# Kernel tuning notes

Measured on AMD Instinct MI355X. Metric: run time of the kernel, lower is better.

Reference implementation:

```python
import jax, jax.numpy as jnp
import numpy as np

D = 512      # input_size == per-head embed_size (wide attention)
H = 8        # num_attn_heads


def setup_inputs() -> dict:
    key = jax.random.key(0)
    ks = jax.random.split(key, 8)
    B, S = 2, 2048
    scale = 1.0 / np.sqrt(D)
    return {
        "Xin_q": jax.random.normal(ks[0], (B, S, D), dtype=jnp.float32),
        "Xin_k": jax.random.normal(ks[1], (B, S, D), dtype=jnp.float32),
        "Xin_v": jax.random.normal(ks[2], (B, S, D), dtype=jnp.float32),
        # per-head projection weights, stored as [H, D_in, D_out] (bias-free)
        "Wq": jax.random.normal(ks[3], (H, D, D), dtype=jnp.float32) * scale,
        "Wk": jax.random.normal(ks[4], (H, D, D), dtype=jnp.float32) * scale,
        "Wv": jax.random.normal(ks[5], (H, D, D), dtype=jnp.float32) * scale,
        # output projection: concat(H*D) -> D, with bias
        "Wz": jax.random.normal(ks[6], (H * D, D), dtype=jnp.float32) * (1.0 / np.sqrt(H * D)),
        "bz": jax.random.normal(ks[7], (D,), dtype=jnp.float32) * 0.01,
    }


def reference(Xin_q, Xin_k, Xin_v, Wq, Wk, Wv, Wz, bz):
    B, Sq, _ = Xin_q.shape
    inv4 = 1.0 / (D ** 0.25)  # each of Q and K scaled by embed_size**(1/4)
    # project all heads at once: [B,H,S,D]
    q = jnp.einsum("bsd,hde->bhse", Xin_q, Wq) * inv4
    k = jnp.einsum("bsd,hde->bhse", Xin_k, Wk) * inv4
    v = jnp.einsum("bsd,hde->bhse", Xin_v, Wv)
    attn = jax.nn.softmax(jnp.einsum("bhqe,bhke->bhqk", q, k), axis=-1)
    z = jnp.einsum("bhqk,bhke->bhqe", attn, v)        # [B,H,S,D]
    # concat heads along last dim (head-major order matches torch.cat over the head loop)
    z = jnp.transpose(z, (0, 2, 1, 3)).reshape(B, Sq, H * D)
    out = z @ Wz + bz                                  # [B,S,D]
    attn_avg = jnp.mean(attn, axis=1)                  # [B,Sq,Skv]
    return out, attn_avg
```

## Files before the change

kernel.cpp:

```cpp
#include <hip/hip_runtime.h>
#include <math.h>

#define BB 2
#define SS 2048
#define D_ 512
#define H_ 8
#define MS (BB * SS)
#define HD (H_ * D_)

typedef short bf16x8 __attribute__((ext_vector_type(8)));
typedef float f32x4 __attribute__((ext_vector_type(4)));

__device__ inline unsigned short f2bf(float f) {
    union { float f; unsigned u; } x{f};
    unsigned r = x.u + 0x7fff + ((x.u >> 16) & 1);
    return (unsigned short)(r >> 16);
}
__device__ inline float bf2f(unsigned short u) {
    union { unsigned u; float f; } x{(unsigned)u << 16};
    return x.f;
}

constexpr size_t SZ_X   = (size_t)MS * D_ * 2;
constexpr size_t SZ_W   = (size_t)H_ * D_ * D_ * 2;
constexpr size_t SZ_WZ  = (size_t)HD * D_ * 2;
constexpr size_t SZ_QK  = (size_t)H_ * MS * D_ * 2;
constexpr size_t SZ_SC  = (size_t)H_ * BB * SS * SS * 2;
constexpr size_t SZ_Z   = (size_t)MS * HD * 2;
constexpr size_t SZ_OP  = (size_t)2 * MS * D_ * 4;
constexpr size_t SZ_LV  = (size_t)H_ * BB * SS * 4;
constexpr size_t OFF_XQ  = 0;
constexpr size_t OFF_XK  = OFF_XQ + SZ_X;
constexpr size_t OFF_XV  = OFF_XK + SZ_X;
constexpr size_t OFF_WQT = OFF_XV + SZ_X;
constexpr size_t OFF_WKT = OFF_WQT + SZ_W;
constexpr size_t OFF_WVT = OFF_WKT + SZ_W;
constexpr size_t OFF_WZT = OFF_WVT + SZ_W;
constexpr size_t OFF_QB  = OFF_WZT + SZ_WZ;
constexpr size_t OFF_KB  = OFF_QB + SZ_QK;
constexpr size_t OFF_VT  = OFF_KB + SZ_QK;
constexpr size_t OFF_SC  = OFF_VT + SZ_QK;
constexpr size_t OFF_Z   = OFF_SC + SZ_SC;
constexpr size_t OFF_OP  = OFF_Z + SZ_Z;
constexpr size_t OFF_LV  = OFF_OP + SZ_OP;
constexpr size_t WS_TOTAL = OFF_LV + SZ_LV;
__device__ __align__(256) unsigned char g_ws[WS_TOTAL];

__device__ inline void gl2lds16(const unsigned short* g, unsigned short* l) {
    __builtin_amdgcn_global_load_lds(
        (const __attribute__((address_space(1))) void*)g,
        (__attribute__((address_space(3))) void*)l, 16, 0, 0);
}

#define BAR() __builtin_amdgcn_s_barrier()
#define PRIO1() __builtin_amdgcn_s_setprio(1)
#define PRIO0() __builtin_amdgcn_s_setprio(0)
#define VMW4() asm volatile("s_waitcnt vmcnt(4)" ::: "memory")
#define VMW0() asm volatile("s_waitcnt vmcnt(0)" ::: "memory")

__device__ __forceinline__ void rd_a(const unsigned short* p, int qm, int o0, int o1,
                                     bf16x8 (&Af)[8]) {
#pragma unroll
    for (int fi = 0; fi < 4; fi++) {
        Af[2 * fi]     = *(const bf16x8*)(p + (qm * 64 + fi * 16) * 64 + o0);
        Af[2 * fi + 1] = *(const bf16x8*)(p + (qm * 64 + fi * 16) * 64 + o1);
    }
}
__device__ __forceinline__ void rd_b(const unsigned short* p, int qn, int o0, int o1,
                                     bf16x8 (&Bf)[4]) {
#pragma unroll
    for (int fj = 0; fj < 2; fj++) {
        Bf[2 * fj]     = *(const bf16x8*)(p + (qn * 32 + fj * 16) * 64 + o0);
        Bf[2 * fj + 1] = *(const bf16x8*)(p + (qn * 32 + fj * 16) * 64 + o1);
    }
}
__device__ __forceinline__ void mma_q(int qm, int qn, const bf16x8 (&Af)[8],
                                      const bf16x8 (&Bf)[4], f32x4 (&acc)[8][4]) {
#pragma unroll
    for (int fi = 0; fi < 4; fi++)
#pragma unroll
        for (int fj = 0; fj < 2; fj++) {
            acc[qm * 4 + fi][qn * 2 + fj] = __builtin_amdgcn_mfma_f32_16x16x32_bf16(
                Af[2 * fi], Bf[2 * fj], acc[qm * 4 + fi][qn * 2 + fj], 0, 0, 0);
            acc[qm * 4 + fi][qn * 2 + fj] = __builtin_amdgcn_mfma_f32_16x16x32_bf16(
                Af[2 * fi + 1], Bf[2 * fj + 1], acc[qm * 4 + fi][qn * 2 + fj], 0, 0, 0);
        }
}

__global__ __launch_bounds__(512, 2) void gemm256_k(
    const unsigned short* __restrict__ A, const unsigned short* __restrict__ B,
    unsigned short* __restrict__ C, int K, int ldA, int ldB, int ldC,
    long sA1, long sA2, long sB1, long sB2, long sC1, long sC2, int d2,
    float alpha, int doExp, const float* __restrict__ rowScale, long sR1, long sR2)
{
    __shared__ unsigned short LA[2][256 * 64];
    __shared__ unsigned short LB[2][256 * 64];
    const int gx = gridDim.x, gy = gridDim.y, gz = gridDim.z;
    int bx, by, bz;
    if (((gy * gz) & 7) == 0) {
        const long L = blockIdx.x + (long)gx * (blockIdx.y + (long)gy * blockIdx.z);
        const int d = (int)(L & 7);
        const long s = L >> 3;
        bx = (int)(s % gx);
        const long yz = d + 8 * (s / gx);
        by = (int)(yz % gy);
        bz = (int)(yz / gy);
    } else {
        bx = blockIdx.x; by = blockIdx.y; bz = blockIdx.z;
    }
    const int z1 = bz / d2, z2 = bz % d2;
    A += z1 * sA1 + z2 * sA2;
    B += z1 * sB1 + z2 * sB2;
    const long cOff = z1 * sC1 + z2 * sC2;
    const long rsOff = z1 * sR1 + z2 * sR2;
    const int m0 = by * 256, n0 = bx * 256;
    const int tid = threadIdx.x;
    const int w = tid >> 6, l = tid & 63;
    const int wm = w >> 2, wn = w & 3;

    const int sr = l >> 3;
    const int sq = (l & 7) ^ sr;
    const unsigned short* gA = A + (long)(m0 + w * 16 + sr) * ldA + sq * 8;
    const unsigned short* gB = B + (long)(n0 + w * 16 + sr) * ldB + sq * 8;

    const int q = l >> 4, sl = l & 7;
    const int o0 = (q ^ sl) * 8;
    const int o1 = ((q + 4) ^ sl) * 8;
    const unsigned short* pa0 = &LA[0][(wm * 128 + (l & 15)) * 64];
    const unsigned short* pa1 = &LA[1][(wm * 128 + (l & 15)) * 64];
    const unsigned short* pb0 = &LB[0][(wn * 64 + (l & 15)) * 64];
    const unsigned short* pb1 = &LB[1][(wn * 64 + (l & 15)) * 64];

    const int nK2 = K >> 7;
    f32x4 acc[8][4] = {};
    bf16x8 Af[8], Bf0[4], Bf1[4];

#define STG_A(bufi, half, t) do { \
    gl2lds16(gA + (long)((half) * 128) * ldA + (long)(t) * 64, \
             &LA[bufi][((half) * 128 + w * 16) * 64]); \
    gl2lds16(gA + (long)((half) * 128 + 8) * ldA + (long)(t) * 64, \
             &LA[bufi][((half) * 128 + w * 16 + 8) * 64]); } while (0)
#define STG_B(bufi, half, t) do { \
    gl2lds16(gB + (long)((half) * 128) * ldB + (long)(t) * 64, \
             &LB[bufi][((half) * 128 + w * 16) * 64]); \
    gl2lds16(gB + (long)((half) * 128 + 8) * ldB + (long)(t) * 64, \
             &LB[bufi][((half) * 128 + w * 16 + 8) * 64]); } while (0)

    STG_A(0, 0, 0); STG_A(0, 1, 0);
    STG_B(0, 0, 0); STG_B(0, 1, 0);
    STG_B(1, 0, 1); STG_B(1, 1, 1);
    VMW4();
    BAR();

    for (int u = 0; u < nK2; ++u) {
        const int t1 = 2 * u + 1, t2 = 2 * u + 2, t3 = 2 * u + 3;
        const bool have = (u + 1 < nK2);
        rd_a(pa0, 0, o0, o1, Af);
        rd_b(pb0, 0, o0, o1, Bf0);
        STG_A(1, 0, t1);
        BAR(); PRIO1(); mma_q(0, 0, Af, Bf0, acc); PRIO0(); BAR();
        rd_b(pb0, 1, o0, o1, Bf1);
        STG_A(1, 1, t1);
        BAR(); PRIO1(); mma_q(0, 1, Af, Bf1, acc); PRIO0(); BAR();
        rd_a(pa0, 1, o0, o1, Af);
        if (have) STG_B(0, 0, t2);
        BAR(); PRIO1(); mma_q(1, 1, Af, Bf1, acc); PRIO0(); BAR();
        if (have) STG_B(0, 1, t2);
        BAR(); PRIO1(); mma_q(1, 0, Af, Bf0, acc); PRIO0();
        if (have) VMW4(); else VMW0();
        BAR();
        rd_a(pa1, 0, o0, o1, Af);
        rd_b(pb1, 0, o0, o1, Bf0);
        if (have) STG_A(0, 0, t2);
        BAR(); PRIO1(); mma_q(0, 0, Af, Bf0, acc); PRIO0(); BAR();
        rd_b(pb1, 1, o0, o1, Bf1);
        if (have) STG_A(0, 1, t2);
        BAR(); PRIO1(); mma_q(0, 1, Af, Bf1, acc); PRIO0(); BAR();
        rd_a(pa1, 1, o0, o1, Af);
        if (have) STG_B(1, 0, t3);
        BAR(); PRIO1(); mma_q(1, 1, Af, Bf1, acc); PRIO0(); BAR();
        if (have) STG_B(1, 1, t3);
        BAR(); PRIO1(); mma_q(1, 0, Af, Bf0, acc); PRIO0();
        if (have) VMW4(); else VMW0();
        BAR();
    }
#undef STG_A
#undef STG_B

    const int rowB = m0 + wm * 128 + q * 4;
    const int colB = n0 + wn * 64 + (l & 15);
    unsigned short* Cp = C + cOff;
#pragma unroll
    for (int mi = 0; mi < 8; mi++) {
#pragma unroll
        for (int rg = 0; rg < 4; rg++) {
            const int row = rowB + mi * 16 + rg;
            const float rs = rowScale ? rowScale[rsOff + row] : 1.0f;
#pragma unroll
            for (int nj = 0; nj < 4; nj++) {
                float v = alpha * acc[mi][nj][rg];
                if (doExp) v = __expf(v);
                Cp[(long)row * ldC + colB + nj * 16] = f2bf(v * rs);
            }
        }
    }
}

__global__ __launch_bounds__(256) void gemm_bt_k(
    const unsigned short* __restrict__ A, const unsigned short* __restrict__ B,
    void* __restrict__ Cv, int K, int ldA, int ldB, int ldC,
    long sA1, long sA2, long sB1, long sB2, long sC1, long sC2, int d2,
    float alpha, const float* __restrict__ bias, int outBf16, int doExp,
    const float* __restrict__ rowScale, long sR1, long sR2)
{
    __shared__ unsigned short As[128 * 64];
    __shared__ unsigned short Bs[128 * 64];
    const int gx = gridDim.x, gy = gridDim.y, gz = gridDim.z;
    int bx, by, bz;
    if (((gy * gz) & 7) == 0) {
        const long L = blockIdx.x + (long)gx * (blockIdx.y + (long)gy * blockIdx.z);
        const int d = (int)(L & 7);
        const long s = L >> 3;
        bx = (int)(s % gx);
        const long yz = d + 8 * (s / gx);
        by = (int)(yz % gy);
        bz = (int)(yz / gy);
    } else {
        bx = blockIdx.x; by = blockIdx.y; bz = blockIdx.z;
    }
    const int z1 = bz / d2, z2 = bz % d2;
    A += z1 * sA1 + z2 * sA2;
    B += z1 * sB1 + z2 * sB2;
    const long cOff = z1 * sC1 + z2 * sC2;
    const long rsOff = z1 * sR1 + z2 * sR2;
    const int m0 = by * 128, n0 = bx * 128;
    const int tid = threadIdx.x;
    const int w = tid >> 6, l = tid & 63;

    const int sr = l >> 3;
    const int sq = (l & 7) ^ sr;
    const unsigned short* ga = A + (long)(m0 + w * 32 + sr) * ldA + sq * 8;
    const unsigned short* gb = B + (long)(n0 + w * 32 + sr) * ldB + sq * 8;
    unsigned short* laA = As + w * 2048;
    unsigned short* laB = Bs + w * 2048;

    const int wm = w >> 1, wn = w & 1;
    const int q = l >> 4;
    const int sl = l & 7;
    const int mA = wm * 64 + (l & 15);
    const int nB = wn * 64 + (l & 15);
    const int s0 = ((q) ^ sl) * 8;
    const int s1 = ((q + 4) ^ sl) * 8;
    const unsigned short* pa0 = As + mA * 64 + s0;
    const unsigned short* pa1 = As + mA * 64 + s1;
    const unsigned short* pb0 = Bs + nB * 64 + s0;
    const unsigned short* pb1 = Bs + nB * 64 + s1;

    f32x4 acc[4][4] = {};
    for (int kk = 0; kk < K; kk += 64) {
#pragma unroll
        for (int i = 0; i < 4; i++) {
            gl2lds16(ga + (long)i * 8 * ldA, laA + i * 512);
            gl2lds16(gb + (long)i * 8 * ldB, laB + i * 512);
        }
        ga += 64; gb += 64;
        __syncthreads();
        bf16x8 af[4], bf[4];
#pragma unroll
        for (int i = 0; i < 4; i++) {
            af[i] = *(const bf16x8*)(pa0 + i * 1024);
            bf[i] = *(const bf16x8*)(pb0 + i * 1024);
        }
#pragma unroll
        for (int mi = 0; mi < 4; mi++)
#pragma unroll
            for (int ni = 0; ni < 4; ni++)
                acc[mi][ni] = __builtin_amdgcn_mfma_f32_16x16x32_bf16(
                    af[mi], bf[ni], acc[mi][ni], 0, 0, 0);
#pragma unroll
        for (int i = 0; i < 4; i++) {
            af[i] = *(const bf16x8*)(pa1 + i * 1024);
            bf[i] = *(const bf16x8*)(pb1 + i * 1024);
        }
#pragma unroll
        for (int mi = 0; mi < 4; mi++)
#pragma unroll
            for (int ni = 0; ni < 4; ni++)
                acc[mi][ni] = __builtin_amdgcn_mfma_f32_16x16x32_bf16(
                    af[mi], bf[ni], acc[mi][ni], 0, 0, 0);
        __syncthreads();
    }

    const int rowB = m0 + wm * 64 + q * 4;
    const int colB = n0 + wn * 64 + (l & 15);
    if (outBf16) {
        unsigned short* C = (unsigned short*)Cv + cOff;
#pragma unroll
        for (int mi = 0; mi < 4; mi++) {
#pragma unroll
            for (int rg = 0; rg < 4; rg++) {
                const int row = rowB + mi * 16 + rg;
                const float rs = rowScale ? rowScale[rsOff + row] : 1.0f;
#pragma unroll
                for (int ni = 0; ni < 4; ni++) {
                    float v = alpha * acc[mi][ni][rg];
                    if (doExp) v = __expf(v);
                    C[(long)row * ldC + colB + ni * 16] = f2bf(v * rs);
                }
            }
        }
    } else {
        float* C = (float*)Cv + cOff;
#pragma unroll
        for (int ni = 0; ni < 4; ni++) {
            const int col = colB + ni * 16;
            const float bs = bias ? bias[col] : 0.f;
#pragma unroll
            for (int mi = 0; mi < 4; mi++)
#pragma unroll
                for (int rg = 0; rg < 4; rg++)
                    C[(long)(rowB + mi * 16 + rg) * ldC + col] =
                        alpha * acc[mi][ni][rg] + bs;
        }
    }
}

__global__ __launch_bounds__(256) void cvt3_k(
    const float* __restrict__ i0, const float* __restrict__ i1, const float* __restrict__ i2,
    unsigned short* __restrict__ o0, unsigned short* __restrict__ o1,
    unsigned short* __restrict__ o2, long n4)
{
    const float* in = blockIdx.z == 0 ? i0 : (blockIdx.z == 1 ? i1 : i2);
    unsigned short* out = blockIdx.z == 0 ? o0 : (blockIdx.z == 1 ? o1 : o2);
    long i = (long)blockIdx.x * 256 + threadIdx.x;
    if (i >= n4) return;
    float4 v = ((const float4*)in)[i];
    ushort4 o;
    o.x = f2bf(v.x); o.y = f2bf(v.y); o.z = f2bf(v.z); o.w = f2bf(v.w);
    ((ushort4*)out)[i] = o;
}

__global__ __launch_bounds__(256) void transcvt3_k(
    const float* __restrict__ i0, const float* __restrict__ i1, const float* __restrict__ i2,
    unsigned short* __restrict__ o0, unsigned short* __restrict__ o1,
    unsigned short* __restrict__ o2)
{
    __shared__ float t[32][33];
    const int zt = blockIdx.z >> 3, h = blockIdx.z & 7;
    const float* in = (zt == 0 ? i0 : (zt == 1 ? i1 : i2)) + (long)h * D_ * D_;
    unsigned short* out = (zt == 0 ? o0 : (zt == 1 ? o1 : o2)) + (long)h * D_ * D_;
    const int r0 = blockIdx.y * 32, c0 = blockIdx.x * 32;
    const int tr = threadIdx.x >> 5, tc = threadIdx.x & 31;
#pragma unroll
    for (int i = 0; i < 4; i++)
        t[tr + i * 8][tc] = in[(long)(r0 + tr + i * 8) * D_ + c0 + tc];
    __syncthreads();
#pragma unroll
    for (int i = 0; i < 4; i++)
        out[(long)(c0 + tr + i * 8) * D_ + r0 + tc] = f2bf(t[tc][tr + i * 8]);
}

__global__ __launch_bounds__(256) void transcvt_k(
    const float* __restrict__ in, unsigned short* __restrict__ out, int R, int C)
{
    __shared__ float t[32][33];
    const int r0 = blockIdx.y * 32, c0 = blockIdx.x * 32;
    const int tr = threadIdx.x >> 5, tc = threadIdx.x & 31;
#pragma unroll
    for (int i = 0; i < 4; i++)
        t[tr + i * 8][tc] = in[(long)(r0 + tr + i * 8) * C + c0 + tc];
    __syncthreads();
#pragma unroll
    for (int i = 0; i < 4; i++)
        out[(long)(c0 + tr + i * 8) * R + r0 + tc] = f2bf(t[tc][tr + i * 8]);
}

__device__ inline float wred_sum(float v) {
#pragma unroll
    for (int o = 32; o; o >>= 1) v += __shfl_down(v, o);
    return v;
}
__global__ __launch_bounds__(256) void sumavg_k(
    const unsigned short* __restrict__ E, float* __restrict__ avg,
    float* __restrict__ linv)
{
    const int blk = blockIdx.x;
    const int b = blk >> 11, s = blk & (SS - 1);
    const int tid = threadIdx.x;
    __shared__ float red[4];
    float av[8] = {};
    const int t0 = tid * 8;
    for (int h = 0; h < H_; h++) {
        const long rowOff = ((long)(h * BB + b) * SS + s) * SS + t0;
        const ushort4 u0 = *(const ushort4*)(E + rowOff);
        const ushort4 u1 = *(const ushort4*)(E + rowOff + 4);
        float vals[8] = {bf2f(u0.x), bf2f(u0.y), bf2f(u0.z), bf2f(u0.w),
                         bf2f(u1.x), bf2f(u1.y), bf2f(u1.z), bf2f(u1.w)};
        float sum = 0.f;
#pragma unroll
        for (int i = 0; i < 8; i++) sum += vals[i];
        float wsum = wred_sum(sum);
        if ((tid & 63) == 0) red[tid >> 6] = wsum;
        __syncthreads();
        sum = red[0] + red[1] + red[2] + red[3];
        __syncthreads();
        const float inv = 1.0f / sum;
        if (tid == 0) linv[(long)(h * BB + b) * SS + s] = inv;
        const float invH = inv * 0.125f;
#pragma unroll
        for (int i = 0; i < 8; i++) av[i] += vals[i] * invH;
    }
    const long aOff = ((long)b * SS + s) * SS + t0;
    float4 a0 = {av[0], av[1], av[2], av[3]};
    float4 a1 = {av[4], av[5], av[6], av[7]};
    *(float4*)(avg + aOff) = a0;
    *(float4*)(avg + aOff + 4) = a1;
}

__global__ __launch_bounds__(256) void addbias_k(
    const float* __restrict__ p0, const float* __restrict__ p1,
    const float* __restrict__ bz, float* __restrict__ out)
{
    const long n4 = (long)MS * D_ / 4;
    long i = (long)blockIdx.x * 256 + threadIdx.x;
    if (i >= n4) return;
    const int col4 = (int)((i * 4) & (D_ - 1));
    float4 a = ((const float4*)p0)[i];
    float4 b = ((const float4*)p1)[i];
    float4 c = *(const float4*)(bz + col4);
    float4 o = {a.x + b.x + c.x, a.y + b.y + c.y, a.z + b.z + c.z, a.w + b.w + c.w};
    ((float4*)out)[i] = o;
}

extern "C" void kernel_launch(void* const* d_in, const int* in_sizes, int n_in,
                              void* d_out, int out_size, void* d_ws, size_t ws_size,
                              hipStream_t stream)
{
    const float* Xq = (const float*)d_in[0];
    const float* Xk = (const float*)d_in[1];
    const float* Xv = (const float*)d_in[2];
    const float* Wq = (const float*)d_in[3];
    const float* Wk = (const float*)d_in[4];
    const float* Wv = (const float*)d_in[5];
    const float* Wz = (const float*)d_in[6];
    const float* bz = (const float*)d_in[7];

    float* out      = (float*)d_out;
    float* attn_avg = out + (long)MS * D_;

    unsigned char* ws = nullptr;
    (void)hipGetSymbolAddress((void**)&ws, HIP_SYMBOL(g_ws));
    unsigned short* Xbq = (unsigned short*)(ws + OFF_XQ);
    unsigned short* Xbk = (unsigned short*)(ws + OFF_XK);
    unsigned short* Xbv = (unsigned short*)(ws + OFF_XV);
    unsigned short* Wqt = (unsigned short*)(ws + OFF_WQT);
    unsigned short* Wkt = (unsigned short*)(ws + OFF_WKT);
    unsigned short* Wvt = (unsigned short*)(ws + OFF_WVT);
    unsigned short* Wzt = (unsigned short*)(ws + OFF_WZT);
    unsigned short* qb  = (unsigned short*)(ws + OFF_QB);
    unsigned short* vT  = (unsigned short*)(ws + OFF_VT);
    unsigned short* scb = (unsigned short*)(ws + OFF_SC);
    unsigned short* zal = (unsigned short*)(ws + OFF_Z);
    float*          opp = (float*)(ws + OFF_OP);
    float*          linv = (float*)(ws + OFF_LV);

    const float inv4 = 1.0f / powf((float)D_, 0.25f);

    const long n4x = (long)MS * D_ / 4;
    cvt3_k<<<dim3((n4x + 255) / 256, 1, 3), 256, 0, stream>>>(
        Xq, Xk, Xv, Xbq, Xbk, Xbv, n4x);
    transcvt3_k<<<dim3(16, 16, 24), 256, 0, stream>>>(Wq, Wk, Wv, Wqt, Wkt, Wvt);
    transcvt_k<<<dim3(16, 128, 1), 256, 0, stream>>>(Wz, Wzt, HD, D_);

    gemm256_k<<<dim3(2, 16, 16), 512, 0, stream>>>(
        Xbq, Wqt, qb, D_, D_, D_, D_,
        (long)MS * D_, 0, (long)H_ * D_ * D_, (long)D_ * D_,
        (long)H_ * MS * D_, (long)MS * D_, 8, inv4, 0, nullptr, 0, 0);
    gemm256_k<<<dim3(8, 2, 16), 512, 0, stream>>>(
        Wvt, Xbv, vT, D_, D_, D_, SS,
        (long)D_ * D_, 0, 0, (long)SS * D_, (long)2 * D_ * SS, (long)D_ * SS, 2,
        1.0f, 0, nullptr, 0, 0);

    gemm256_k<<<dim3(8, 8, 16), 512, 0, stream>>>(
        qb, qb + (long)H_ * MS * D_, scb, D_, D_, D_, SS,
        (long)MS * D_, (long)SS * D_, (long)MS * D_, (long)SS * D_,
        (long)2 * SS * SS, (long)SS * SS, 2, 1.0f, 1, nullptr, 0, 0);

    sumavg_k<<<dim3(BB * SS), 256, 0, stream>>>(scb, attn_avg, linv);

    gemm256_k<<<dim3(2, 8, 16), 512, 0, stream>>>(
        scb, vT, zal, SS, SS, SS, HD,
        (long)2 * SS * SS, (long)SS * SS, (long)2 * D_ * SS, (long)D_ * SS,
        512, (long)SS * HD, 2, 1.0f, 0,
        linv, (long)BB * SS, (long)SS);

    gemm_bt_k<<<dim3(4, 32, 2), 256, 0, stream>>>(
        zal, Wzt, opp, HD / 2, HD, HD, D_,
        0, 2048, 0, 2048, 0, (long)MS * D_, 2, 1.0f, nullptr, 0, 0, nullptr, 0, 0);
    const long n4o = (long)MS * D_ / 4;
    addbias_k<<<dim3((n4o + 255) / 256), 256, 0, stream>>>(
        opp, opp + (long)MS * D_, bz, out);
}
```

Before: 476.1 us.

## Double-buffer GEMM register fragments to overlap LDS reads with MFMA

Splits the A and B register fragments into two sets each, so LDS reads for the next quarter-tile are issued before the current MFMA block. The first fragments are prefetched before the loop and the next iteration's are loaded at the end. Each phase now has one barrier instead of two, and sched_barrier fences keep the compiler from reordering across phases. The aim is to hide LDS latency and cut barrier stalls, at the cost of more VGPRs, which could reduce occupancy, and a more delicate barrier ordering around buffer reuse.

```diff
diff --git a/kernel.cpp b/kernel.cpp
--- a/kernel.cpp
+++ b/kernel.cpp
@@ -55,6 +55,7 @@
 #define BAR() __builtin_amdgcn_s_barrier()
 #define PRIO1() __builtin_amdgcn_s_setprio(1)
 #define PRIO0() __builtin_amdgcn_s_setprio(0)
+#define SCHED0() __builtin_amdgcn_sched_barrier(0)
 #define VMW4() asm volatile("s_waitcnt vmcnt(4)" ::: "memory")
 #define VMW0() asm volatile("s_waitcnt vmcnt(0)" ::: "memory")
 
@@ -133,7 +134,7 @@
 
     const int nK2 = K >> 7;
     f32x4 acc[8][4] = {};
-    bf16x8 Af[8], Bf0[4], Bf1[4];
+    bf16x8 AfX[8], AfY[8], BfP[4], BfQ[4];
 
 #define STG_A(bufi, half, t) do { \
     gl2lds16(gA + (long)((half) * 128) * ldA + (long)(t) * 64, \
@@ -151,37 +152,55 @@
     STG_B(1, 0, 1); STG_B(1, 1, 1);
     VMW4();
     BAR();
+    rd_a(pa0, 0, o0, o1, AfX);
+    rd_b(pb0, 0, o0, o1, BfP);
 
     for (int u = 0; u < nK2; ++u) {
         const int t1 = 2 * u + 1, t2 = 2 * u + 2, t3 = 2 * u + 3;
         const bool have = (u + 1 < nK2);
-        rd_a(pa0, 0, o0, o1, Af);
-        rd_b(pb0, 0, o0, o1, Bf0);
+        rd_b(pb0, 1, o0, o1, BfQ);
         STG_A(1, 0, t1);
-        BAR(); PRIO1(); mma_q(0, 0, Af, Bf0, acc); PRIO0(); BAR();
-        rd_b(pb0, 1, o0, o1, Bf1);
+        SCHED0();
+        PRIO1(); mma_q(0, 0, AfX, BfP, acc); PRIO0();
+        BAR();
+        rd_a(pa0, 1, o0, o1, AfY);
         STG_A(1, 1, t1);
-        BAR(); PRIO1(); mma_q(0, 1, Af, Bf1, acc); PRIO0(); BAR();
-        rd_a(pa0, 1, o0, o1, Af);
+        SCHED0();
+        PRIO1(); mma_q(0, 1, AfX, BfQ, acc); PRIO0();
+        BAR();
         if (have) STG_B(0, 0, t2);
-        BAR(); PRIO1(); mma_q(1, 1, Af, Bf1, acc); PRIO0(); BAR();
+        SCHED0();
+        PRIO1(); mma_q(1, 1, AfY, BfQ, acc); PRIO0();
+        BAR();
         if (have) STG_B(0, 1, t2);
-        BAR(); PRIO1(); mma_q(1, 0, Af, Bf0, acc); PRIO0();
         if (have) VMW4(); else VMW0();
         BAR();
-        rd_a(pa1, 0, o0, o1, Af);
-        rd_b(pb1, 0, o0, o1, Bf0);
+        rd_a(pa1, 0, o0, o1, AfX);
+        SCHED0();
+        PRIO1(); mma_q(1, 0, AfY, BfP, acc); PRIO0();
+        rd_b(pb1, 0, o0, o1, BfP);
+        BAR();
+        rd_b(pb1, 1, o0, o1, BfQ);
         if (have) STG_A(0, 0, t2);
-        BAR(); PRIO1(); mma_q(0, 0, Af, Bf0, acc); PRIO0(); BAR();
-        rd_b(pb1, 1, o0, o1, Bf1);
+        SCHED0();
+        PRIO1(); mma_q(0, 0, AfX, BfP, acc); PRIO0();
+        BAR();
+        rd_a(pa1, 1, o0, o1, AfY);
         if (have) STG_A(0, 1, t2);
-        BAR(); PRIO1(); mma_q(0, 1, Af, Bf1, acc); PRIO0(); BAR();
-        rd_a(pa1, 1, o0, o1, Af);
+        SCHED0();
+        PRIO1(); mma_q(0, 1, AfX, BfQ, acc); PRIO0();
+        BAR();
         if (have) STG_B(1, 0, t3);
-        BAR(); PRIO1(); mma_q(1, 1, Af, Bf1, acc); PRIO0(); BAR();
+        SCHED0();
+        PRIO1(); mma_q(1, 1, AfY, BfQ, acc); PRIO0();
+        BAR();
         if (have) STG_B(1, 1, t3);
-        BAR(); PRIO1(); mma_q(1, 0, Af, Bf0, acc); PRIO0();
         if (have) VMW4(); else VMW0();
+        BAR();
+        if (have) rd_a(pa0, 0, o0, o1, AfX);
+        SCHED0();
+        PRIO1(); mma_q(1, 0, AfY, BfP, acc); PRIO0();
+        if (have) rd_b(pb0, 0, o0, o1, BfP);
         BAR();
     }
 #undef STG_A
```

Result: slower. 489.1 us (+2.7%).

## Make 256x256 GEMM persistent with XCD-aware tile assignment and cross-tile prefetch

Applied to the files above, without the earlier changes.

The 256x256 bf16 GEMM kernel becomes persistent. It launches 256 blocks, and each block walks tiles strided by 32 within a z-slice group pinned to one XCD (blockIdx & 7). In the last K iteration it stages the next tile's first A/B chunks into LDS, so the next tile's loads overlap the current tile's final MFMAs and epilogue. This removes per-block launch and prologue bubbles and keeps each batch's data in one XCD's L2. The cost is that the epilogue stores are now serialized inside the block and load balance depends on the tile count per XCD.

```diff
diff --git a/kernel.cpp b/kernel.cpp
--- a/kernel.cpp
+++ b/kernel.cpp
@@ -91,38 +91,17 @@
     const unsigned short* __restrict__ A, const unsigned short* __restrict__ B,
     unsigned short* __restrict__ C, int K, int ldA, int ldB, int ldC,
     long sA1, long sA2, long sB1, long sB2, long sC1, long sC2, int d2,
-    float alpha, int doExp, const float* __restrict__ rowScale, long sR1, long sR2)
+    float alpha, int doExp, const float* __restrict__ rowScale, long sR1, long sR2,
+    int gx, int gy, int gz)
 {
     __shared__ unsigned short LA[2][256 * 64];
     __shared__ unsigned short LB[2][256 * 64];
-    const int gx = gridDim.x, gy = gridDim.y, gz = gridDim.z;
-    int bx, by, bz;
-    if (((gy * gz) & 7) == 0) {
-        const long L = blockIdx.x + (long)gx * (blockIdx.y + (long)gy * blockIdx.z);
-        const int d = (int)(L & 7);
-        const long s = L >> 3;
-        bx = (int)(s % gx);
-        const long yz = d + 8 * (s / gx);
-        by = (int)(yz % gy);
-        bz = (int)(yz / gy);
-    } else {
-        bx = blockIdx.x; by = blockIdx.y; bz = blockIdx.z;
-    }
-    const int z1 = bz / d2, z2 = bz % d2;
-    A += z1 * sA1 + z2 * sA2;
-    B += z1 * sB1 + z2 * sB2;
-    const long cOff = z1 * sC1 + z2 * sC2;
-    const long rsOff = z1 * sR1 + z2 * sR2;
-    const int m0 = by * 256, n0 = bx * 256;
     const int tid = threadIdx.x;
     const int w = tid >> 6, l = tid & 63;
     const int wm = w >> 2, wn = w & 3;
 
     const int sr = l >> 3;
     const int sq = (l & 7) ^ sr;
-    const unsigned short* gA = A + (long)(m0 + w * 16 + sr) * ldA + sq * 8;
-    const unsigned short* gB = B + (long)(n0 + w * 16 + sr) * ldB + sq * 8;
-
     const int q = l >> 4, sl = l & 7;
     const int o0 = (q ^ sl) * 8;
     const int o1 = ((q + 4) ^ sl) * 8;
@@ -131,79 +110,124 @@
     const unsigned short* pb0 = &LB[0][(wn * 64 + (l & 15)) * 64];
     const unsigned short* pb1 = &LB[1][(wn * 64 + (l & 15)) * 64];
 
+    const int tilesPerZ = gx * gy;
+    const int zPerXcd = gz >> 3;
+    const int perXcd = zPerXcd * tilesPerZ;
+    const int xcd = blockIdx.x & 7, jj = blockIdx.x >> 3;
+    const int nT = (perXcd - jj + 31) >> 5;
     const int nK2 = K >> 7;
+
+    auto decode = [&](int idx, const unsigned short*& gA, const unsigned short*& gB,
+                      long& cO, long& rO, int& m0o, int& n0o) {
+        const int zl = idx / tilesPerZ;
+        const int rem = idx - zl * tilesPerZ;
+        const int by = rem / gx;
+        const int bx = rem - by * gx;
+        const int bz = xcd * zPerXcd + zl;
+        const int z1 = bz / d2, z2 = bz - z1 * d2;
+        m0o = by * 256; n0o = bx * 256;
+        gA = A + z1 * sA1 + z2 * sA2 + (long)(m0o + w * 16 + sr) * ldA + sq * 8;
+        gB = B + z1 * sB1 + z2 * sB2 + (long)(n0o + w * 16 + sr) * ldB + sq * 8;
+        cO = z1 * sC1 + z2 * sC2;
+        rO = z1 * sR1 + z2 * sR2;
+    };
+
+    const unsigned short *gAc, *gBc, *gAn, *gBn;
+    long cOff, rsOff, cOffN, rsOffN;
+    int m0, n0, m0N, n0N;
+    decode(jj, gAc, gBc, cOff, rsOff, m0, n0);
+    gAn = gAc; gBn = gBc; cOffN = cOff; rsOffN = rsOff; m0N = m0; n0N = n0;
+
     f32x4 acc[8][4] = {};
     bf16x8 Af[8], Bf0[4], Bf1[4];
 
-#define STG_A(bufi, half, t) do { \
-    gl2lds16(gA + (long)((half) * 128) * ldA + (long)(t) * 64, \
+#define STG_A(bufi, half, base, t) do { \
+    gl2lds16((base) + (long)((half) * 128) * ldA + (long)(t) * 64, \
              &LA[bufi][((half) * 128 + w * 16) * 64]); \
-    gl2lds16(gA + (long)((half) * 128 + 8) * ldA + (long)(t) * 64, \
+    gl2lds16((base) + (long)((half) * 128 + 8) * ldA + (long)(t) * 64, \
              &LA[bufi][((half) * 128 + w * 16 + 8) * 64]); } while (0)
-#define STG_B(bufi, half, t) do { \
-    gl2lds16(gB + (long)((half) * 128) * ldB + (long)(t) * 64, \
+#define STG_B(bufi, half, base, t) do { \
+    gl2lds16((base) + (long)((half) * 128) * ldB + (long)(t) * 64, \
              &LB[bufi][((half) * 128 + w * 16) * 64]); \
-    gl2lds16(gB + (long)((half) * 128 + 8) * ldB + (long)(t) * 64, \
+    gl2lds16((base) + (long)((half) * 128 + 8) * ldB + (long)(t) * 64, \
              &LB[bufi][((half) * 128 + w * 16 + 8) * 64]); } while (0)
 
-    STG_A(0, 0, 0); STG_A(0, 1, 0);
-    STG_B(0, 0, 0); STG_B(0, 1, 0);
-    STG_B(1, 0, 1); STG_B(1, 1, 1);
+    STG_A(0, 0, gAc, 0); STG_A(0, 1, gAc, 0);
+    STG_B(0, 0, gBc, 0); STG_B(0, 1, gBc, 0);
+    STG_B(1, 0, gBc, 1); STG_B(1, 1, gBc, 1);
     VMW4();
     BAR();
 
-    for (int u = 0; u < nK2; ++u) {
-        const int t1 = 2 * u + 1, t2 = 2 * u + 2, t3 = 2 * u + 3;
-        const bool have = (u + 1 < nK2);
-        rd_a(pa0, 0, o0, o1, Af);
-        rd_b(pb0, 0, o0, o1, Bf0);
-        STG_A(1, 0, t1);
-        BAR(); PRIO1(); mma_q(0, 0, Af, Bf0, acc); PRIO0(); BAR();
-        rd_b(pb0, 1, o0, o1, Bf1);
-        STG_A(1, 1, t1);
-        BAR(); PRIO1(); mma_q(0, 1, Af, Bf1, acc); PRIO0(); BAR();
-        rd_a(pa0, 1, o0, o1, Af);
-        if (have) STG_B(0, 0, t2);
-        BAR(); PRIO1(); mma_q(1, 1, Af, Bf1, acc); PRIO0(); BAR();
-        if (have) STG_B(0, 1, t2);
-        BAR(); PRIO1(); mma_q(1, 0, Af, Bf0, acc); PRIO0();
-        if (have) VMW4(); else VMW0();
-        BAR();
-        rd_a(pa1, 0, o0, o1, Af);
-        rd_b(pb1, 0, o0, o1, Bf0);
-        if (have) STG_A(0, 0, t2);
-        BAR(); PRIO1(); mma_q(0, 0, Af, Bf0, acc); PRIO0(); BAR();
-        rd_b(pb1, 1, o0, o1, Bf1);
-        if (have) STG_A(0, 1, t2);
-        BAR(); PRIO1(); mma_q(0, 1, Af, Bf1, acc); PRIO0(); BAR();
-        rd_a(pa1, 1, o0, o1, Af);
-        if (have) STG_B(1, 0, t3);
-        BAR(); PRIO1(); mma_q(1, 1, Af, Bf1, acc); PRIO0(); BAR();
-        if (have) STG_B(1, 1, t3);
-        BAR(); PRIO1(); mma_q(1, 0, Af, Bf0, acc); PRIO0();
-        if (have) VMW4(); else VMW0();
-        BAR();
+    for (int k = 0; k < nT; ++k) {
+        const bool hasNext = (k + 1 < nT);
+        if (hasNext) decode(jj + (k + 1) * 32, gAn, gBn, cOffN, rsOffN, m0N, n0N);
+
+        for (int u = 0; u < nK2; ++u) {
+            const int t1 = 2 * u + 1, t2 = 2 * u + 2, t3 = 2 * u + 3;
+            const bool lastU = (u == nK2 - 1);
+            const bool stg = !lastU || hasNext;
+            const unsigned short* a2 = lastU ? gAn : gAc;
+            const unsigned short* b2 = lastU ? gBn : gBc;
+            const int tt2 = lastU ? 0 : t2;
+            const int tt3 = lastU ? 1 : t3;
+            rd_a(pa0, 0, o0, o1, Af);
+            rd_b(pb0, 0, o0, o1, Bf0);
+            STG_A(1, 0, gAc, t1);
+            BAR(); PRIO1(); mma_q(0, 0, Af, Bf0, acc); PRIO0(); BAR();
+            rd_b(pb0, 1, o0, o1, Bf1);
+            STG_A(1, 1, gAc, t1);
+            BAR(); PRIO1(); mma_q(0, 1, Af, Bf1, acc); PRIO0(); BAR();
+            rd_a(pa0, 1, o0, o1, Af);
+            if (stg) STG_B(0, 0, b2, tt2);
+            BAR(); PRIO1(); mma_q(1, 1, Af, Bf1, acc); PRIO0(); BAR();
+            if (stg) STG_B(0, 1, b2, tt2);
+            BAR(); PRIO1(); mma_q(1, 0, Af, Bf0, acc); PRIO0();
+            if (stg) VMW4(); else VMW0();
+            BAR();
+            rd_a(pa1, 0, o0, o1, Af);
+            rd_b(pb1, 0, o0, o1, Bf0);
+            if (stg) STG_A(0, 0, a2, tt2);
+            BAR(); PRIO1(); mma_q(0, 0, Af, Bf0, acc); PRIO0(); BAR();
+            rd_b(pb1, 1, o0, o1, Bf1);
+            if (stg) STG_A(0, 1, a2, tt2);
+            BAR(); PRIO1(); mma_q(0, 1, Af, Bf1, acc); PRIO0(); BAR();
+            rd_a(pa1, 1, o0, o1, Af);
+            if (stg) STG_B(1, 0, b2, tt3);
+            BAR(); PRIO1(); mma_q(1, 1, Af, Bf1, acc); PRIO0(); BAR();
+            if (stg) STG_B(1, 1, b2, tt3);
+            BAR(); PRIO1(); mma_q(1, 0, Af, Bf0, acc); PRIO0();
+            if (stg) VMW4(); else VMW0();
+            BAR();
+        }
+
+        {
+            const int rowB = m0 + wm * 128 + q * 4;
+            const int colB = n0 + wn * 64 + (l & 15);
+            unsigned short* Cp = C + cOff;
+#pragma unroll
+            for (int mi = 0; mi < 8; mi++) {
+#pragma unroll
+                for (int rg = 0; rg < 4; rg++) {
+                    const int row = rowB + mi * 16 + rg;
+                    const float rs = rowScale ? rowScale[rsOff + row] : 1.0f;
+#pragma unroll
+                    for (int nj = 0; nj < 4; nj++) {
+                        float v = alpha * acc[mi][nj][rg];
+                        if (doExp) v = __expf(v);
+                        Cp[(long)row * ldC + colB + nj * 16] = f2bf(v * rs);
+                    }
+                }
+            }
+        }
+#pragma unroll
+        for (int mi = 0; mi < 8; mi++)
+#pragma unroll
+            for (int nj = 0; nj < 4; nj++)
+                acc[mi][nj] = (f32x4){0.f, 0.f, 0.f, 0.f};
+        gAc = gAn; gBc = gBn; cOff = cOffN; rsOff = rsOffN; m0 = m0N; n0 = n0N;
     }
 #undef STG_A
 #undef STG_B
-
-    const int rowB = m0 + wm * 128 + q * 4;
-    const int colB = n0 + wn * 64 + (l & 15);
-    unsigned short* Cp = C + cOff;
-#pragma unroll
-    for (int mi = 0; mi < 8; mi++) {
-#pragma unroll
-        for (int rg = 0; rg < 4; rg++) {
-            const int row = rowB + mi * 16 + rg;
-            const float rs = rowScale ? rowScale[rsOff + row] : 1.0f;
-#pragma unroll
-            for (int nj = 0; nj < 4; nj++) {
-                float v = alpha * acc[mi][nj][rg];
-                if (doExp) v = __expf(v);
-                Cp[(long)row * ldC + colB + nj * 16] = f2bf(v * rs);
-            }
-        }
-    }
 }
 
 __global__ __launch_bounds__(256) void gemm_bt_k(
@@ -472,27 +496,31 @@
     transcvt3_k<<<dim3(16, 16, 24), 256, 0, stream>>>(Wq, Wk, Wv, Wqt, Wkt, Wvt);
     transcvt_k<<<dim3(16, 128, 1), 256, 0, stream>>>(Wz, Wzt, HD, D_);
 
-    gemm256_k<<<dim3(2, 16, 16), 512, 0, stream>>>(
+    gemm256_k<<<dim3(256), 512, 0, stream>>>(
         Xbq, Wqt, qb, D_, D_, D_, D_,
         (long)MS * D_, 0, (long)H_ * D_ * D_, (long)D_ * D_,
-        (long)H_ * MS * D_, (long)MS * D_, 8, inv4, 0, nullptr, 0, 0);
-    gemm256_k<<<dim3(8, 2, 16), 512, 0, stream>>>(
+        (long)H_ * MS * D_, (long)MS * D_, 8, inv4, 0, nullptr, 0, 0,
+        2, 16, 16);
+    gemm256_k<<<dim3(256), 512, 0, stream>>>(
         Wvt, Xbv, vT, D_, D_, D_, SS,
         (long)D_ * D_, 0, 0, (long)SS * D_, (long)2 * D_ * SS, (long)D_ * SS, 2,
-        1.0f, 0, nullptr, 0, 0);
-
-    gemm256_k<<<dim3(8, 8, 16), 512, 0, stream>>>(
+        1.0f, 0, nullptr, 0, 0,
+        8, 2, 16);
+
+    gemm256_k<<<dim3(256), 512, 0, stream>>>(
         qb, qb + (long)H_ * MS * D_, scb, D_, D_, D_, SS,
         (long)MS * D_, (long)SS * D_, (long)MS * D_, (long)SS * D_,
-        (long)2 * SS * SS, (long)SS * SS, 2, 1.0f, 1, nullptr, 0, 0);
+        (long)2 * SS * SS, (long)SS * SS, 2, 1.0f, 1, nullptr, 0, 0,
+        8, 8, 16);
 
     sumavg_k<<<dim3(BB * SS), 256, 0, stream>>>(scb, attn_avg, linv);
 
-    gemm256_k<<<dim3(2, 8, 16), 512, 0, stream>>>(
+    gemm256_k<<<dim3(256), 512, 0, stream>>>(
         scb, vT, zal, SS, SS, SS, HD,
         (long)2 * SS * SS, (long)SS * SS, (long)2 * D_ * SS, (long)D_ * SS,
         512, (long)SS * HD, 2, 1.0f, 0,
-        linv, (long)BB * SS, (long)SS);
+        linv, (long)BB * SS, (long)SS,
+        2, 8, 16);
 
     gemm_bt_k<<<dim3(4, 32, 2), 256, 0, stream>>>(
         zal, Wzt, opp, HD / 2, HD, HD, D_,
```

Measured after the change: 457.3 us. 1.04x faster.
